# Optimization experiments

Hardware: AMD Instinct MI355X
Metric: run time of the kernel (lower is better)

Reference implementation:

```python
import jax, jax.numpy as jnp
import numpy as np

L, B, S, H = 2, 32, 2048, 512  # layers, batch, src_len, hidden_size
D = 2 * H                      # feature dim of hidden / encoder_outputs


def setup_inputs() -> dict:
    key = jax.random.key(0)
    k1, k2, k3, k4, k5 = jax.random.split(key, 5)
    scale = 1.0 / np.sqrt(4 * H)
    return {
        "hidden": jax.random.normal(k1, (L, B, D), dtype=jnp.float32),
        "encoder_outputs": jax.random.normal(k2, (B, S, D), dtype=jnp.float32),
        "attn_w": jax.random.normal(k3, (H, 4 * H), dtype=jnp.float32) * scale,
        "attn_b": jax.random.normal(k4, (H,), dtype=jnp.float32) * scale,
        "v_w": jax.random.normal(k5, (1, H), dtype=jnp.float32) * (1.0 / np.sqrt(H)),
    }


def reference(hidden, encoder_outputs, attn_w, attn_b, v_w):
    # hidden: [L, B, D]; permute(1,0,2) then [:, -1, :] == last layer state [B, D]
    h = hidden[-1]  # [B, D]
    # Avoid materializing the [B,S,2D] concat: split attn_w into the block acting
    # on the (repeated) hidden part and the block acting on encoder_outputs.
    w_h, w_e = attn_w[:, :D], attn_w[:, D:]          # [H, D] each
    # hidden contribution is constant over src_len -> compute once per batch row
    e_h = jnp.einsum('bd,hd->bh', h, w_h)            # [B, H]
    e_e = jnp.einsum('bsd,hd->bsh', encoder_outputs, w_e)  # [B, S, H]
    energy = jnp.tanh(e_e + e_h[:, None, :] + attn_b)      # [B, S, H]
    scores = jnp.einsum('bsh,h->bs', energy, v_w[0])       # [B, S]
    attention_weights = jax.nn.softmax(scores, axis=1)     # [B, S]
    context = jnp.einsum('bs,bsd->bd', attention_weights, encoder_outputs)
    return (context[:, None, :], attention_weights[:, None, :])
```

## Files before the change

### kernel.cpp

```cpp
#include <hip/hip_runtime.h>
#include <math.h>

#define LL 2
#define BB 32
#define SS 2048
#define HH 512
#define DD 1024
#define W4S 2048

#define BM 64
#define BN 256
#define BK 64
#define NT (DD / BK)
#define ASTR 72

typedef __attribute__((ext_vector_type(8))) short bf16x8;
typedef __attribute__((ext_vector_type(4))) float f32x4;

__device__ inline unsigned pk2_rne(float a, float b) {
    unsigned ua = __float_as_uint(a), ub = __float_as_uint(b);
    unsigned ra = (ua + 0x7fffu + ((ua >> 16) & 1u)) >> 16;
    unsigned rb = (ub + 0x7fffu + ((ub >> 16) & 1u)) & 0xffff0000u;
    return ra | rb;
}

__device__ inline unsigned pk2_hu(float a, float b) {
    unsigned ua = __float_as_uint(a) + 0x8000u;
    unsigned ub = __float_as_uint(b) + 0x8000u;
    return __builtin_amdgcn_perm(ub, ua, 0x07060302u);
}

__device__ inline float fast_tanh(float x) {
    x = fminf(9.f, fmaxf(-9.f, x));
    float e = __expf(2.f * x);
    return 1.f - 2.f * __builtin_amdgcn_rcpf(e + 1.f);
}

__device__ inline void gl_lds16(const unsigned short* g, short* l) {
    __builtin_amdgcn_global_load_lds(
        (const __attribute__((address_space(1))) unsigned int*)g,
        (__attribute__((address_space(3))) unsigned int*)l, 16, 0, 0);
}

__global__ void k_zero(float* __restrict__ scores) {
    scores[blockIdx.x * 256 + threadIdx.x] = 0.f;
}

__global__ __launch_bounds__(256) void k_pack(const float* __restrict__ attn_w,
                                              unsigned short* __restrict__ Bp) {
    int h = blockIdx.x, t = threadIdx.x;
    float4 v = *(const float4*)(attn_w + (size_t)h * W4S + DD + t * 4);
    uint2 r = make_uint2(pk2_rne(v.x, v.y), pk2_rne(v.z, v.w));
    *(uint2*)(Bp + (size_t)h * DD + t * 4) = r;
}

__global__ __launch_bounds__(256) void k_base(const float* __restrict__ hidden,
                                              const float* __restrict__ attn_w,
                                              const float* __restrict__ attn_b,
                                              float* __restrict__ base) {
    int wid  = (blockIdx.x * 256 + threadIdx.x) >> 6;
    int lane = threadIdx.x & 63;
    int b = wid >> 9;
    int h = wid & (HH - 1);
    const float4* h4 = (const float4*)(hidden + (size_t)(LL - 1) * BB * DD + (size_t)b * DD);
    const float4* w4 = (const float4*)(attn_w + (size_t)h * W4S);
    float s = 0.f;
    #pragma unroll
    for (int i = 0; i < 4; i++) {
        float4 a = h4[lane + i * 64], w = w4[lane + i * 64];
        s += a.x * w.x + a.y * w.y + a.z * w.z + a.w * w.w;
    }
    #pragma unroll
    for (int off = 32; off; off >>= 1) s += __shfl_xor(s, off);
    if (lane == 0) base[b * HH + h] = s + attn_b[h];
}

__global__ __launch_bounds__(256, 2) void k_scores(const float* __restrict__ enc,
                                                   const unsigned short* __restrict__ Bp,
                                                   const float* __restrict__ base,
                                                   const float* __restrict__ vw,
                                                   float* __restrict__ scores) {
    __shared__ short As[BM * ASTR];
    __shared__ short Bs[2][BN * BK];

    const int tid  = threadIdx.x;
    const int wid  = tid >> 6;
    const int lane = tid & 63;
    const int lm   = lane & 15;
    const int kq   = lane >> 4;
    const int n0   = blockIdx.x * BN;
    const int m0   = blockIdx.y * BM;
    const int b    = m0 >> 11;
    const int wn   = wid * 64;

    const int rowA = tid >> 3;
    const int gA   = tid & 7;
    const float* Ag0 = enc + (size_t)(m0 + rowA) * DD + gA * 8;
    const float* Ag1 = Ag0 + (size_t)32 * DD;
    short* AsW0 = As + rowA * ASTR + gA * 8;
    short* AsW1 = AsW0 + 32 * ASTR;

    const int brow = lane >> 3;
    const int bgsw = (lane & 7) ^ brow;
    const unsigned short* Bg = Bp + (size_t)(n0 + wn + brow) * DD + bgsw * 8;

    f32x4 acc[4][4];
    #pragma unroll
    for (int i = 0; i < 4; i++)
        #pragma unroll
        for (int j = 0; j < 4; j++) acc[i][j] = (f32x4){0.f, 0.f, 0.f, 0.f};

    #pragma unroll
    for (int i = 0; i < 8; i++)
        gl_lds16(Bg + (size_t)(i * 8) * DD, &Bs[0][(wn + i * 8) * BK]);
    float4 a0 = *(const float4*)(Ag0);
    float4 a1 = *(const float4*)(Ag0 + 4);
    float4 a2 = *(const float4*)(Ag1);
    float4 a3 = *(const float4*)(Ag1 + 4);

    for (int kt = 0; kt < NT; kt++) {
        __syncthreads();
        uint4 p0 = {pk2_hu(a0.x, a0.y), pk2_hu(a0.z, a0.w),
                    pk2_hu(a1.x, a1.y), pk2_hu(a1.z, a1.w)};
        uint4 p1 = {pk2_hu(a2.x, a2.y), pk2_hu(a2.z, a2.w),
                    pk2_hu(a3.x, a3.y), pk2_hu(a3.z, a3.w)};
        *(uint4*)AsW0 = p0;
        *(uint4*)AsW1 = p1;
        __syncthreads();
        if (kt + 1 < NT) {
            #pragma unroll
            for (int i = 0; i < 8; i++)
                gl_lds16(Bg + (size_t)(i * 8) * DD + (kt + 1) * BK,
                         &Bs[(kt + 1) & 1][(wn + i * 8) * BK]);
            a0 = *(const float4*)(Ag0 + (kt + 1) * BK);
            a1 = *(const float4*)(Ag0 + (kt + 1) * BK + 4);
            a2 = *(const float4*)(Ag1 + (kt + 1) * BK);
            a3 = *(const float4*)(Ag1 + (kt + 1) * BK + 4);
        }
        const short* Bb = Bs[kt & 1];
        #pragma unroll
        for (int s = 0; s < 2; s++) {
            bf16x8 af[4];
            #pragma unroll
            for (int mi = 0; mi < 4; mi++)
                af[mi] = *(const bf16x8*)&As[(mi * 16 + lm) * ASTR + (s * 4 + kq) * 8];
            #pragma unroll
            for (int ni = 0; ni < 4; ni++) {
                bf16x8 bf = *(const bf16x8*)
                    &Bb[(wn + ni * 16 + lm) * BK + (((s * 4 + kq)) ^ (lm & 7)) * 8];
                #pragma unroll
                for (int mi = 0; mi < 4; mi++)
                    acc[mi][ni] = __builtin_amdgcn_mfma_f32_16x16x32_bf16(
                        af[mi], bf, acc[mi][ni], 0, 0, 0);
            }
        }
    }

    const float* basep = base + b * HH + n0 + wn;
    const float* vp    = vw + n0 + wn;
    float p[4][4] = {};
    #pragma unroll
    for (int ni = 0; ni < 4; ni++) {
        int nl = ni * 16 + lm;
        float bs = basep[nl];
        float vv = vp[nl];
        #pragma unroll
        for (int mi = 0; mi < 4; mi++)
            #pragma unroll
            for (int r = 0; r < 4; r++)
                p[mi][r] += vv * fast_tanh(acc[mi][ni][r] + bs);
    }
    #pragma unroll
    for (int off = 8; off; off >>= 1)
        #pragma unroll
        for (int mi = 0; mi < 4; mi++)
            #pragma unroll
            for (int r = 0; r < 4; r++)
                p[mi][r] += __shfl_xor(p[mi][r], off);
    if (lm == 0) {
        #pragma unroll
        for (int mi = 0; mi < 4; mi++)
            #pragma unroll
            for (int r = 0; r < 4; r++)
                atomicAdd(&scores[m0 + mi * 16 + kq * 4 + r], p[mi][r]);
    }
}

__global__ __launch_bounds__(256) void k_softmax(const float* __restrict__ scores,
                                                 float* __restrict__ wout) {
    int b = blockIdx.x, tid = threadIdx.x;
    const float* rowp = scores + b * SS;
    float v[8];
    float m = -1e30f;
    #pragma unroll
    for (int i = 0; i < 8; i++) { v[i] = rowp[tid + i * 256]; m = fmaxf(m, v[i]); }
    __shared__ float sm[4], ssum[4];
    #pragma unroll
    for (int off = 32; off; off >>= 1) m = fmaxf(m, __shfl_xor(m, off));
    if ((tid & 63) == 0) sm[tid >> 6] = m;
    __syncthreads();
    m = fmaxf(fmaxf(sm[0], sm[1]), fmaxf(sm[2], sm[3]));
    float s = 0.f;
    #pragma unroll
    for (int i = 0; i < 8; i++) { v[i] = __expf(v[i] - m); s += v[i]; }
    #pragma unroll
    for (int off = 32; off; off >>= 1) s += __shfl_xor(s, off);
    if ((tid & 63) == 0) ssum[tid >> 6] = s;
    __syncthreads();
    s = ssum[0] + ssum[1] + ssum[2] + ssum[3];
    float inv = 1.f / s;
    #pragma unroll
    for (int i = 0; i < 8; i++) wout[b * SS + tid + i * 256] = v[i] * inv;
}

#define CCH 64
__global__ __launch_bounds__(256) void k_ctxpart(const float* __restrict__ enc,
                                                 const float* __restrict__ w,
                                                 float* __restrict__ part) {
    int b = blockIdx.x, c = blockIdx.y, tid = threadIdx.x;
    __shared__ float wsh[CCH];
    if (tid < CCH) wsh[tid] = w[b * SS + c * CCH + tid];
    __syncthreads();
    const float4* e4 = (const float4*)(enc + ((size_t)b * SS + c * CCH) * DD);
    float4 acc = {0.f, 0.f, 0.f, 0.f};
    #pragma unroll 8
    for (int s = 0; s < CCH; s++) {
        float wv  = wsh[s];
        float4 ev = e4[(size_t)s * (DD / 4) + tid];
        acc.x += wv * ev.x; acc.y += wv * ev.y;
        acc.z += wv * ev.z; acc.w += wv * ev.w;
    }
    *(float4*)(part + (size_t)(b * 32 + c) * DD + tid * 4) = acc;
}

__global__ __launch_bounds__(256) void k_ctxreduce(const float* __restrict__ part,
                                                   float* __restrict__ ctx) {
    int b = blockIdx.x, d = blockIdx.y * 256 + threadIdx.x;
    float s = 0.f;
    #pragma unroll
    for (int c = 0; c < 32; c++) s += part[(size_t)(b * 32 + c) * DD + d];
    ctx[b * DD + d] = s;
}

extern "C" void kernel_launch(void* const* d_in, const int* in_sizes, int n_in,
                              void* d_out, int out_size, void* d_ws, size_t ws_size,
                              hipStream_t stream) {
    const float* hidden = (const float*)d_in[0];
    const float* enc    = (const float*)d_in[1];
    const float* attn_w = (const float*)d_in[2];
    const float* attn_b = (const float*)d_in[3];
    const float* v_w    = (const float*)d_in[4];

    float* out      = (float*)d_out;
    float* ctx_out  = out;
    float* attn_out = out + BB * DD;

    float* base   = (float*)d_ws;
    float* scores = base + BB * HH;
    unsigned short* Bp = (unsigned short*)(scores + BB * SS);
    float* part   = (float*)(Bp + (size_t)HH * DD);

    hipLaunchKernelGGL(k_zero, dim3(BB * SS / 256), dim3(256), 0, stream, scores);
    hipLaunchKernelGGL(k_pack, dim3(HH), dim3(256), 0, stream, attn_w, Bp);
    hipLaunchKernelGGL(k_base, dim3(BB * HH / 4), dim3(256), 0, stream,
                       hidden, attn_w, attn_b, base);
    hipLaunchKernelGGL(k_scores, dim3(2, BB * SS / BM), dim3(256), 0, stream,
                       enc, Bp, base, v_w, scores);
    hipLaunchKernelGGL(k_softmax, dim3(BB), dim3(256), 0, stream, scores, attn_out);
    hipLaunchKernelGGL(k_ctxpart, dim3(BB, SS / CCH), dim3(256), 0, stream,
                       enc, attn_out, part);
    hipLaunchKernelGGL(k_ctxreduce, dim3(BB, DD / 256), dim3(256), 0, stream,
                       part, ctx_out);
}
```

Measured before the change: 477.6 us.

## Fuse softmax numerator and context partials into scores kernel with full-H tiles

The scores GEMM now covers all 512 hidden columns per block (BM=128, BN=512, 512 threads), so each block reduces its scores inside LDS instead of using atomics. It then computes the unnormalised softmax numerator exp(score) without subtracting a row maximum, accumulates the per-batch denominator atomically, and immediately forms context partials from the encoder rows it just streamed, while they are likely still cached. A final kernel divides both the context and the attention weights by the denominator. This removes the zero, softmax and separate context passes, along with a second full read of encoder_outputs from memory. The cost is a much larger LDS footprint (about 146KB per block, so likely one block per CU) and reliance on a clamp at 80 instead of a max-subtraction, which assumes scores stay small.

```diff
diff --git a/kernel.cpp b/kernel.cpp
--- a/kernel.cpp
+++ b/kernel.cpp
@@ -8,8 +8,8 @@
 #define DD 1024
 #define W4S 2048
 
-#define BM 64
-#define BN 256
+#define BM 128
+#define BN 512
 #define BK 64
 #define NT (DD / BK)
 #define ASTR 72
@@ -42,13 +42,11 @@
         (__attribute__((address_space(3))) unsigned int*)l, 16, 0, 0);
 }
 
-__global__ void k_zero(float* __restrict__ scores) {
-    scores[blockIdx.x * 256 + threadIdx.x] = 0.f;
-}
-
 __global__ __launch_bounds__(256) void k_pack(const float* __restrict__ attn_w,
-                                              unsigned short* __restrict__ Bp) {
+                                              unsigned short* __restrict__ Bp,
+                                              float* __restrict__ den) {
     int h = blockIdx.x, t = threadIdx.x;
+    if (h == 0 && t < BB) den[t] = 0.f;
     float4 v = *(const float4*)(attn_w + (size_t)h * W4S + DD + t * 4);
     uint2 r = make_uint2(pk2_rne(v.x, v.y), pk2_rne(v.z, v.w));
     *(uint2*)(Bp + (size_t)h * DD + t * 4) = r;
@@ -75,11 +73,13 @@
     if (lane == 0) base[b * HH + h] = s + attn_b[h];
 }
 
-__global__ __launch_bounds__(256, 2) void k_scores(const float* __restrict__ enc,
+__global__ __launch_bounds__(512, 2) void k_scores(const float* __restrict__ enc,
                                                    const unsigned short* __restrict__ Bp,
                                                    const float* __restrict__ base,
                                                    const float* __restrict__ vw,
-                                                   float* __restrict__ scores) {
+                                                   float* __restrict__ den,
+                                                   float* __restrict__ part,
+                                                   float* __restrict__ attn_out) {
     __shared__ short As[BM * ASTR];
     __shared__ short Bs[2][BN * BK];
 
@@ -88,27 +88,29 @@
     const int lane = tid & 63;
     const int lm   = lane & 15;
     const int kq   = lane >> 4;
-    const int n0   = blockIdx.x * BN;
-    const int m0   = blockIdx.y * BM;
+    const int wr   = wid >> 2;
+    const int wc   = wid & 3;
+    const int m0   = blockIdx.x * BM;
     const int b    = m0 >> 11;
+    const int srow = m0 & (SS - 1);
     const int wn   = wid * 64;
 
     const int rowA = tid >> 3;
     const int gA   = tid & 7;
     const float* Ag0 = enc + (size_t)(m0 + rowA) * DD + gA * 8;
-    const float* Ag1 = Ag0 + (size_t)32 * DD;
+    const float* Ag1 = Ag0 + (size_t)64 * DD;
     short* AsW0 = As + rowA * ASTR + gA * 8;
-    short* AsW1 = AsW0 + 32 * ASTR;
+    short* AsW1 = AsW0 + 64 * ASTR;
 
     const int brow = lane >> 3;
     const int bgsw = (lane & 7) ^ brow;
-    const unsigned short* Bg = Bp + (size_t)(n0 + wn + brow) * DD + bgsw * 8;
-
-    f32x4 acc[4][4];
+    const unsigned short* Bg = Bp + (size_t)(wn + brow) * DD + bgsw * 8;
+
+    f32x4 acc[4][8];
     #pragma unroll
     for (int i = 0; i < 4; i++)
         #pragma unroll
-        for (int j = 0; j < 4; j++) acc[i][j] = (f32x4){0.f, 0.f, 0.f, 0.f};
+        for (int j = 0; j < 8; j++) acc[i][j] = (f32x4){0.f, 0.f, 0.f, 0.f};
 
     #pragma unroll
     for (int i = 0; i < 8; i++)
@@ -143,11 +145,11 @@
             bf16x8 af[4];
             #pragma unroll
             for (int mi = 0; mi < 4; mi++)
-                af[mi] = *(const bf16x8*)&As[(mi * 16 + lm) * ASTR + (s * 4 + kq) * 8];
-            #pragma unroll
-            for (int ni = 0; ni < 4; ni++) {
+                af[mi] = *(const bf16x8*)&As[(wr * 64 + mi * 16 + lm) * ASTR + (s * 4 + kq) * 8];
+            #pragma unroll
+            for (int ni = 0; ni < 8; ni++) {
                 bf16x8 bf = *(const bf16x8*)
-                    &Bb[(wn + ni * 16 + lm) * BK + (((s * 4 + kq)) ^ (lm & 7)) * 8];
+                    &Bb[(wc * 128 + ni * 16 + lm) * BK + (((s * 4 + kq)) ^ (lm & 7)) * 8];
                 #pragma unroll
                 for (int mi = 0; mi < 4; mi++)
                     acc[mi][ni] = __builtin_amdgcn_mfma_f32_16x16x32_bf16(
@@ -156,11 +158,16 @@
         }
     }
 
-    const float* basep = base + b * HH + n0 + wn;
-    const float* vp    = vw + n0 + wn;
+    __syncthreads();
+    float* red  = (float*)As;
+    float* esh  = red + 4 * BM;
+    float* dsum = esh + BM;
+
+    const float* basep = base + b * HH + wc * 128;
+    const float* vp    = vw + wc * 128;
     float p[4][4] = {};
     #pragma unroll
-    for (int ni = 0; ni < 4; ni++) {
+    for (int ni = 0; ni < 8; ni++) {
         int nl = ni * 16 + lm;
         float bs = basep[nl];
         float vv = vp[nl];
@@ -182,64 +189,53 @@
         for (int mi = 0; mi < 4; mi++)
             #pragma unroll
             for (int r = 0; r < 4; r++)
-                atomicAdd(&scores[m0 + mi * 16 + kq * 4 + r], p[mi][r]);
-    }
-}
-
-__global__ __launch_bounds__(256) void k_softmax(const float* __restrict__ scores,
-                                                 float* __restrict__ wout) {
-    int b = blockIdx.x, tid = threadIdx.x;
-    const float* rowp = scores + b * SS;
-    float v[8];
-    float m = -1e30f;
-    #pragma unroll
-    for (int i = 0; i < 8; i++) { v[i] = rowp[tid + i * 256]; m = fmaxf(m, v[i]); }
-    __shared__ float sm[4], ssum[4];
-    #pragma unroll
-    for (int off = 32; off; off >>= 1) m = fmaxf(m, __shfl_xor(m, off));
-    if ((tid & 63) == 0) sm[tid >> 6] = m;
+                red[wc * BM + wr * 64 + mi * 16 + kq * 4 + r] = p[mi][r];
+    }
     __syncthreads();
-    m = fmaxf(fmaxf(sm[0], sm[1]), fmaxf(sm[2], sm[3]));
-    float s = 0.f;
-    #pragma unroll
-    for (int i = 0; i < 8; i++) { v[i] = __expf(v[i] - m); s += v[i]; }
-    #pragma unroll
-    for (int off = 32; off; off >>= 1) s += __shfl_xor(s, off);
-    if ((tid & 63) == 0) ssum[tid >> 6] = s;
+    if (tid < BM) {
+        float s = red[tid] + red[BM + tid] + red[2 * BM + tid] + red[3 * BM + tid];
+        s = fminf(s, 80.f);
+        float e = __expf(s);
+        attn_out[b * SS + srow + tid] = e;
+        esh[tid] = e;
+        float rs = e;
+        #pragma unroll
+        for (int off = 32; off; off >>= 1) rs += __shfl_xor(rs, off);
+        if ((tid & 63) == 0) dsum[tid >> 6] = rs;
+    }
     __syncthreads();
-    s = ssum[0] + ssum[1] + ssum[2] + ssum[3];
-    float inv = 1.f / s;
-    #pragma unroll
-    for (int i = 0; i < 8; i++) wout[b * SS + tid + i * 256] = v[i] * inv;
-}
-
-#define CCH 64
-__global__ __launch_bounds__(256) void k_ctxpart(const float* __restrict__ enc,
-                                                 const float* __restrict__ w,
-                                                 float* __restrict__ part) {
-    int b = blockIdx.x, c = blockIdx.y, tid = threadIdx.x;
-    __shared__ float wsh[CCH];
-    if (tid < CCH) wsh[tid] = w[b * SS + c * CCH + tid];
-    __syncthreads();
-    const float4* e4 = (const float4*)(enc + ((size_t)b * SS + c * CCH) * DD);
-    float4 acc = {0.f, 0.f, 0.f, 0.f};
+    if (tid == 0) atomicAdd(den + b, dsum[0] + dsum[1]);
+
+    const int half = tid >> 8;
+    const int c4   = tid & 255;
+    const float4* e4 = (const float4*)(enc + (size_t)(m0 + half * 64) * DD) + c4;
+    float4 a = {0.f, 0.f, 0.f, 0.f};
     #pragma unroll 8
-    for (int s = 0; s < CCH; s++) {
-        float wv  = wsh[s];
-        float4 ev = e4[(size_t)s * (DD / 4) + tid];
-        acc.x += wv * ev.x; acc.y += wv * ev.y;
-        acc.z += wv * ev.z; acc.w += wv * ev.w;
-    }
-    *(float4*)(part + (size_t)(b * 32 + c) * DD + tid * 4) = acc;
-}
-
-__global__ __launch_bounds__(256) void k_ctxreduce(const float* __restrict__ part,
-                                                   float* __restrict__ ctx) {
-    int b = blockIdx.x, d = blockIdx.y * 256 + threadIdx.x;
-    float s = 0.f;
-    #pragma unroll
-    for (int c = 0; c < 32; c++) s += part[(size_t)(b * 32 + c) * DD + d];
-    ctx[b * DD + d] = s;
+    for (int j = 0; j < 64; j++) {
+        float w = esh[half * 64 + j];
+        float4 ev = e4[(size_t)j * (DD / 4)];
+        a.x += w * ev.x; a.y += w * ev.y;
+        a.z += w * ev.z; a.w += w * ev.w;
+    }
+    *(float4*)(part + (size_t)(blockIdx.x * 2 + half) * DD + c4 * 4) = a;
+}
+
+__global__ __launch_bounds__(256) void k_finish(const float* __restrict__ part,
+                                                const float* __restrict__ den,
+                                                float* __restrict__ ctx,
+                                                float* __restrict__ attn) {
+    int b = blockIdx.x, y = blockIdx.y, t = threadIdx.x;
+    float inv = 1.f / den[b];
+    if (y < 4) {
+        int d = y * 256 + t;
+        float s = 0.f;
+        #pragma unroll
+        for (int j = 0; j < 32; j++) s += part[(size_t)(b * 32 + j) * DD + d];
+        ctx[b * DD + d] = s * inv;
+    } else {
+        int sid = (y - 4) * 256 + t;
+        attn[b * SS + sid] *= inv;
+    }
 }
 
 extern "C" void kernel_launch(void* const* d_in, const int* in_sizes, int n_in,
@@ -255,20 +251,16 @@
     float* ctx_out  = out;
     float* attn_out = out + BB * DD;
 
-    float* base   = (float*)d_ws;
-    float* scores = base + BB * HH;
-    unsigned short* Bp = (unsigned short*)(scores + BB * SS);
-    float* part   = (float*)(Bp + (size_t)HH * DD);
-
-    hipLaunchKernelGGL(k_zero, dim3(BB * SS / 256), dim3(256), 0, stream, scores);
-    hipLaunchKernelGGL(k_pack, dim3(HH), dim3(256), 0, stream, attn_w, Bp);
+    float* base = (float*)d_ws;
+    float* den  = base + BB * HH;
+    unsigned short* Bp = (unsigned short*)(den + 64);
+    float* part = (float*)(Bp + (size_t)HH * DD);
+
+    hipLaunchKernelGGL(k_pack, dim3(HH), dim3(256), 0, stream, attn_w, Bp, den);
     hipLaunchKernelGGL(k_base, dim3(BB * HH / 4), dim3(256), 0, stream,
                        hidden, attn_w, attn_b, base);
-    hipLaunchKernelGGL(k_scores, dim3(2, BB * SS / BM), dim3(256), 0, stream,
-                       enc, Bp, base, v_w, scores);
-    hipLaunchKernelGGL(k_softmax, dim3(BB), dim3(256), 0, stream, scores, attn_out);
-    hipLaunchKernelGGL(k_ctxpart, dim3(BB, SS / CCH), dim3(256), 0, stream,
-                       enc, attn_out, part);
-    hipLaunchKernelGGL(k_ctxreduce, dim3(BB, DD / 256), dim3(256), 0, stream,
-                       part, ctx_out);
-}
+    hipLaunchKernelGGL(k_scores, dim3(BB * SS / BM), dim3(512), 0, stream,
+                       enc, Bp, base, v_w, den, part, attn_out);
+    hipLaunchKernelGGL(k_finish, dim3(BB, 12), dim3(256), 0, stream,
+                       part, den, ctx_out, attn_out);
+}
```

Result: faster. 462.6 us (-3.1%).
